# Kernel optimization log

Measured on AMD Instinct MI355X. Metric: run time of the kernel, lower is better.

The kernel has to match this reference:

```python
import jax, jax.numpy as jnp
import numpy as np

DIM = 1024
N_HEADS = 16
HEAD_DIM = DIM // N_HEADS
SCALE = 1.0 / HEAD_DIM ** 0.5


def setup_inputs() -> dict:
    key = jax.random.key(0)
    k1, k2, k3, k4, k5 = jax.random.split(key, 5)
    B, T = 4, 2048
    x = jax.random.normal(k1, (B, T, DIM), dtype=jnp.float32)
    # torch nn.Linear weights: y = x @ W.T + b
    w_qkv = jax.random.normal(k2, (3 * DIM, DIM), dtype=jnp.float32) * 0.02
    b_qkv = jax.random.normal(k3, (3 * DIM,), dtype=jnp.float32) * 0.02
    w_proj = jax.random.normal(k4, (DIM, DIM), dtype=jnp.float32) * 0.02
    b_proj = jax.random.normal(k5, (DIM,), dtype=jnp.float32) * 0.02
    return {"x": x, "w_qkv": w_qkv, "b_qkv": b_qkv, "w_proj": w_proj, "b_proj": b_proj}


def reference(x, w_qkv, b_qkv, w_proj, b_proj):
    B, T, D = x.shape
    qkv = x @ w_qkv.T + b_qkv                              # [B, T, 3D]
    qkv = qkv.reshape(B, T, 3, N_HEADS, HEAD_DIM)
    qkv = jnp.transpose(qkv, (2, 0, 3, 1, 4))              # [3, B, h, T, d]
    q, k, v = qkv[0], qkv[1], qkv[2]
    s = jnp.einsum('bhqd,bhkd->bhqk', q, k) * SCALE        # [B, h, T, T]
    attn = jax.nn.softmax(s, axis=-1)
    out = jnp.einsum('bhqk,bhkd->bqhd', attn, v)           # [B, T, h, d]
    out = out.reshape(B, T, D)
    return out @ w_proj.T + b_proj
```

## Files before the change

kernel.cpp:

```cpp
#include <hip/hip_runtime.h>
#include <stdint.h>

typedef short short8 __attribute__((ext_vector_type(8)));
typedef _Float16 half4 __attribute__((ext_vector_type(4)));
typedef _Float16 half8 __attribute__((ext_vector_type(8)));
typedef __fp16 fp16x2 __attribute__((ext_vector_type(2)));
typedef unsigned int uint2v __attribute__((ext_vector_type(2)));
typedef unsigned int uintx4 __attribute__((ext_vector_type(4)));
typedef float floatx4 __attribute__((ext_vector_type(4)));

#define LOG2E 1.44269504088896340736f
#define QSCALE (0.125f * LOG2E)

static __device__ __forceinline__ unsigned short f2bf(float f) {
  unsigned int u = __float_as_uint(f);
  u += 0x7fffu + ((u >> 16) & 1u);
  return (unsigned short)(u >> 16);
}

static __device__ __forceinline__ float fexp2(float x) {
#if __has_builtin(__builtin_amdgcn_exp2f)
  return __builtin_amdgcn_exp2f(x);
#else
  return exp2f(x);
#endif
}

#define GLD_LDS16(gp, lp)                                                      \
  __builtin_amdgcn_global_load_lds(                                            \
      (const __attribute__((address_space(1))) void*)(gp),                     \
      (__attribute__((address_space(3))) void*)(lp), 16, 0, 0)

__global__ __launch_bounds__(256) void cvt_f32_bf16(
    const float* __restrict__ in, unsigned short* __restrict__ out, int n) {
  int i = (blockIdx.x * 256 + threadIdx.x) * 4;
  if (i >= n) return;
  float4 v = *(const float4*)(in + i);
  ushort4 u;
  u.x = f2bf(v.x); u.y = f2bf(v.y); u.z = f2bf(v.z); u.w = f2bf(v.w);
  *(ushort4*)(out + i) = u;
}

template <int MODE>
__global__ __launch_bounds__(256, 2) void gemm_bt(
    const unsigned short* __restrict__ A, const unsigned short* __restrict__ Bm,
    const float* __restrict__ bias, float* __restrict__ outF,
    unsigned short* __restrict__ qo, unsigned short* __restrict__ ko,
    _Float16* __restrict__ vto, int M, int N, int K) {
  __shared__ unsigned short As[128 * 64];
  __shared__ unsigned short Bs[128 * 64];
  const int tid = threadIdx.x;
  const int w = tid >> 6, l = tid & 63;
  const int lr = l & 15, lg = l >> 4;
  const int nbn = N >> 7;
  const int nwg = gridDim.x;
  const int bid = blockIdx.x;
  const int cpx = nwg >> 3;
  const int swz = (bid & 7) * cpx + (bid >> 3);
  const int bm = swz / nbn, bn = swz % nbn;
  const int wm = w >> 1, wn = w & 1;

  floatx4 acc[4][4];
#pragma unroll
  for (int i = 0; i < 4; ++i)
#pragma unroll
    for (int j = 0; j < 4; ++j) acc[i][j] = (floatx4){0.f, 0.f, 0.f, 0.f};

  for (int k0 = 0; k0 < K; k0 += 64) {
#pragma unroll
    for (int i = 0; i < 4; ++i) {
      int c = i * 256 + tid;
      const unsigned short* ga =
          A + ((size_t)bm * 128 + (c >> 3)) * K + k0 + (c & 7) * 8;
      GLD_LDS16(ga, As + (size_t)(i * 256 + w * 64) * 8);
    }
#pragma unroll
    for (int i = 0; i < 4; ++i) {
      int c = i * 256 + tid;
      const unsigned short* gb =
          Bm + ((size_t)bn * 128 + (c >> 3)) * K + k0 + (c & 7) * 8;
      GLD_LDS16(gb, Bs + (size_t)(i * 256 + w * 64) * 8);
    }
    __syncthreads();
#pragma unroll
    for (int kk = 0; kk < 2; ++kk) {
      short8 af[4], bf[4];
#pragma unroll
      for (int i = 0; i < 4; ++i)
        af[i] = *(const short8*)&As[(wm * 64 + i * 16 + lr) * 64 + kk * 32 + lg * 8];
#pragma unroll
      for (int j = 0; j < 4; ++j)
        bf[j] = *(const short8*)&Bs[(wn * 64 + j * 16 + lr) * 64 + kk * 32 + lg * 8];
#pragma unroll
      for (int i = 0; i < 4; ++i)
#pragma unroll
        for (int j = 0; j < 4; ++j)
          acc[i][j] = __builtin_amdgcn_mfma_f32_16x16x32_bf16(af[i], bf[j],
                                                              acc[i][j], 0, 0, 0);
    }
    __syncthreads();
  }

#pragma unroll
  for (int i = 0; i < 4; ++i) {
    int row0 = bm * 128 + wm * 64 + i * 16 + lg * 4;
#pragma unroll
    for (int j = 0; j < 4; ++j) {
      int col = bn * 128 + wn * 64 + j * 16 + lr;
      float bv = bias[col];
#pragma unroll
      for (int jj = 0; jj < 4; ++jj) {
        float v = acc[i][j][jj] + bv;
        int r = row0 + jj;
        if (MODE == 0) {
          outF[(size_t)r * N + col] = v;
        } else {
          int three = col >> 10, cc = col & 1023;
          int h = cc >> 6, d = cc & 63;
          int b = r >> 11, t = r & 2047;
          if (three == 0)
            qo[(((size_t)(b * 16 + h)) * 2048 + t) * 64 + d] = f2bf(v * QSCALE);
          else if (three == 1)
            ko[(((size_t)(b * 16 + h)) * 2048 + t) * 64 + d] = f2bf(v);
          else
            vto[(((size_t)(b * 16 + h)) * 64 + d) * 2048 + t] = (_Float16)v;
        }
      }
    }
  }
}

__global__ __launch_bounds__(256, 3) void attn_fwd(
    const unsigned short* __restrict__ Qg, const unsigned short* __restrict__ Kg,
    const _Float16* __restrict__ VTg, unsigned short* __restrict__ Og) {
  __shared__ unsigned short Ks[2][64 * 64];
  __shared__ _Float16 Vs[2][64 * 64];

  const int bid0 = blockIdx.x;
  const int bid = (bid0 & 7) * 128 + (bid0 >> 3);
  const int bh = bid >> 4, qt = bid & 15;
  const int b = bh >> 4, hh = bh & 15;
  const int tid = threadIdx.x, w = tid >> 6, l = tid & 63;
  const int l4 = l & 15, g = l >> 4;
  const unsigned short* Q = Qg + (size_t)bh * (2048 * 64);
  const unsigned short* Kp = Kg + (size_t)bh * (2048 * 64);
  const _Float16* VT = VTg + (size_t)bh * (64 * 2048);
  const int qw = qt * 128 + w * 32;

  const int r0 = tid >> 3;
  const int s0 = (tid & 7) ^ (r0 & 7);
  const int kv0 = (r0 & 16) ? (((r0 & 15) >> 2) * 8 + 4 + (r0 & 3))
                            : ((r0 >> 2) * 8 + (r0 & 3));
  const unsigned short* kp0 = Kp + (size_t)kv0 * 64 + s0 * 8;
  const unsigned short* kp1 = Kp + (size_t)(kv0 + 32) * 64 + s0 * 8;
  const _Float16* vp0 = VT + (size_t)r0 * 2048 + s0 * 8;
  const _Float16* vp1 = VT + (size_t)(r0 + 32) * 2048 + s0 * 8;
  unsigned short* ksd0 = &Ks[0][tid * 8];
  unsigned short* ksd1 = &Ks[0][(256 + tid) * 8];
  _Float16* vsd0 = &Vs[0][tid * 8];
  _Float16* vsd1 = &Vs[0][(256 + tid) * 8];

#define STAGE(bufofs, tt)                                                     \
  do {                                                                        \
    GLD_LDS16(kp0 + (size_t)(tt) * 64, ksd0 + (bufofs) * 4096);               \
    GLD_LDS16(kp1 + (size_t)(tt) * 64, ksd1 + (bufofs) * 4096);               \
    GLD_LDS16(vp0 + (tt), vsd0 + (bufofs) * 4096);                            \
    GLD_LDS16(vp1 + (tt), vsd1 + (bufofs) * 4096);                            \
  } while (0)

  const int kb0 = l4 * 64 + ((g ^ (l4 & 7)) * 8);
  const int kb1 = l4 * 64 + (((4 + g) ^ (l4 & 7)) * 8);
  int vb[2];
#pragma unroll
  for (int B = 0; B < 2; ++B)
    vb[B] = l4 * 64 + (((B * 4 + g) ^ (l4 & 7)) * 8);

  short8 qf[2][2];
#pragma unroll
  for (int qs = 0; qs < 2; ++qs)
#pragma unroll
    for (int c = 0; c < 2; ++c)
      qf[qs][c] =
          *(const short8*)&Q[(size_t)(qw + qs * 16 + l4) * 64 + c * 32 + g * 8];

  floatx4 o[2][4];
#pragma unroll
  for (int qs = 0; qs < 2; ++qs)
#pragma unroll
    for (int db = 0; db < 4; ++db) o[qs][db] = (floatx4){0.f, 0.f, 0.f, 0.f};
  float m[2] = {-__builtin_inff(), -__builtin_inff()};
  float lp[2] = {0.f, 0.f};

  STAGE(0, 0);
  __syncthreads();

#pragma unroll 2
  for (int it = 0; it < 32; ++it) {
    const int cur = it & 1;
    if (it + 1 < 32) STAGE(cur ^ 1, (it + 1) * 64);

    floatx4 s[2][4];
#pragma unroll
    for (int f = 0; f < 4; ++f) {
      short8 kf0 = *(const short8*)&Ks[cur][kb0 + f * 1024];
      short8 kf1 = *(const short8*)&Ks[cur][kb1 + f * 1024];
      floatx4 z = (floatx4){0.f, 0.f, 0.f, 0.f};
      floatx4 t00 = __builtin_amdgcn_mfma_f32_16x16x32_bf16(kf0, qf[0][0], z, 0, 0, 0);
      s[0][f] = __builtin_amdgcn_mfma_f32_16x16x32_bf16(kf1, qf[0][1], t00, 0, 0, 0);
      floatx4 t10 = __builtin_amdgcn_mfma_f32_16x16x32_bf16(kf0, qf[1][0], z, 0, 0, 0);
      s[1][f] = __builtin_amdgcn_mfma_f32_16x16x32_bf16(kf1, qf[1][1], t10, 0, 0, 0);
    }

    uint2v pu[2][4];
#pragma unroll
    for (int qs = 0; qs < 2; ++qs) {
      float e[16];
      float rs = 0.f;
#pragma unroll
      for (int f = 0; f < 4; ++f)
#pragma unroll
        for (int jj = 0; jj < 4; ++jj) {
          float pv = fexp2(s[qs][f][jj] - m[qs]);
          e[f * 4 + jj] = pv;
          rs += pv;
        }

      if (!__all(rs <= 256.0f)) {
        float a0 = fmaxf(fmaxf(s[qs][0][0], s[qs][0][1]), fmaxf(s[qs][0][2], s[qs][0][3]));
        float a1 = fmaxf(fmaxf(s[qs][1][0], s[qs][1][1]), fmaxf(s[qs][1][2], s[qs][1][3]));
        float a2 = fmaxf(fmaxf(s[qs][2][0], s[qs][2][1]), fmaxf(s[qs][2][2], s[qs][2][3]));
        float a3 = fmaxf(fmaxf(s[qs][3][0], s[qs][3][1]), fmaxf(s[qs][3][2], s[qs][3][3]));
        float pp = fmaxf(fmaxf(a0, a1), fmaxf(a2, a3));
        pp = fmaxf(pp, __shfl_xor(pp, 16));
        pp = fmaxf(pp, __shfl_xor(pp, 32));
        float mo = m[qs];
        m[qs] = fmaxf(mo, pp);
        float al = fexp2(mo - m[qs]);
        lp[qs] *= al;
#pragma unroll
        for (int jj = 0; jj < 4; ++jj) {
          float alr = __shfl(al, g * 4 + jj);
          o[qs][0][jj] *= alr; o[qs][1][jj] *= alr;
          o[qs][2][jj] *= alr; o[qs][3][jj] *= alr;
        }
        rs = 0.f;
#pragma unroll
        for (int f = 0; f < 4; ++f)
#pragma unroll
          for (int jj = 0; jj < 4; ++jj) {
            float pv = fexp2(s[qs][f][jj] - m[qs]);
            e[f * 4 + jj] = pv;
            rs += pv;
          }
      }
      lp[qs] += rs;

#pragma unroll
      for (int f = 0; f < 4; ++f) {
        fp16x2 plo = __builtin_amdgcn_cvt_pkrtz(e[f * 4 + 0], e[f * 4 + 1]);
        fp16x2 phi = __builtin_amdgcn_cvt_pkrtz(e[f * 4 + 2], e[f * 4 + 3]);
        pu[qs][f].x = __builtin_bit_cast(unsigned int, plo);
        pu[qs][f].y = __builtin_bit_cast(unsigned int, phi);
      }
    }

#pragma unroll
    for (int B = 0; B < 2; ++B) {
      uintx4 ua0, ua1;
      ua0.x = pu[0][2 * B].x;     ua0.y = pu[0][2 * B].y;
      ua0.z = pu[0][2 * B + 1].x; ua0.w = pu[0][2 * B + 1].y;
      ua1.x = pu[1][2 * B].x;     ua1.y = pu[1][2 * B].y;
      ua1.z = pu[1][2 * B + 1].x; ua1.w = pu[1][2 * B + 1].y;
      half8 pa0 = __builtin_bit_cast(half8, ua0);
      half8 pa1 = __builtin_bit_cast(half8, ua1);
#pragma unroll
      for (int db = 0; db < 4; ++db) {
        half8 vf = *(const half8*)&Vs[cur][vb[B] + db * 1024];
        o[0][db] = __builtin_amdgcn_mfma_f32_16x16x32_f16(pa0, vf, o[0][db], 0, 0, 0);
        o[1][db] = __builtin_amdgcn_mfma_f32_16x16x32_f16(pa1, vf, o[1][db], 0, 0, 0);
      }
    }
    __syncthreads();
  }

#pragma unroll
  for (int qs = 0; qs < 2; ++qs) {
    float ls = lp[qs];
    ls += __shfl_xor(ls, 16);
    ls += __shfl_xor(ls, 32);
    float invq = 1.f / ls;
    float inv[4];
#pragma unroll
    for (int jj = 0; jj < 4; ++jj) inv[jj] = __shfl(invq, g * 4 + jj);
#pragma unroll
    for (int db = 0; db < 4; ++db)
#pragma unroll
      for (int jj = 0; jj < 4; ++jj)
        Og[((size_t)b * 2048 + qw + qs * 16 + g * 4 + jj) * 1024 + hh * 64 +
           db * 16 + l4] = f2bf(o[qs][db][jj] * inv[jj]);
  }
#undef STAGE
}

extern "C" void kernel_launch(void* const* d_in, const int* in_sizes, int n_in,
                              void* d_out, int out_size, void* d_ws, size_t ws_size,
                              hipStream_t stream) {
  const float* x = (const float*)d_in[0];
  const float* w_qkv = (const float*)d_in[1];
  const float* b_qkv = (const float*)d_in[2];
  const float* w_proj = (const float*)d_in[3];
  const float* b_proj = (const float*)d_in[4];
  float* out = (float*)d_out;

  char* p = (char*)d_ws;
  unsigned short* xb = (unsigned short*)p;     p += (size_t)8192 * 1024 * 2;
  unsigned short* wqkvb = (unsigned short*)p;  p += (size_t)3072 * 1024 * 2;
  unsigned short* wprojb = (unsigned short*)p; p += (size_t)1024 * 1024 * 2;
  unsigned short* qb = (unsigned short*)p;     p += (size_t)64 * 2048 * 64 * 2;
  unsigned short* kb = (unsigned short*)p;     p += (size_t)64 * 2048 * 64 * 2;
  _Float16* vtb = (_Float16*)p;                p += (size_t)64 * 64 * 2048 * 2;
  unsigned short* attnb = (unsigned short*)p;  p += (size_t)8192 * 1024 * 2;

  cvt_f32_bf16<<<dim3(8192), dim3(256), 0, stream>>>(x, xb, 8192 * 1024);
  cvt_f32_bf16<<<dim3(3072), dim3(256), 0, stream>>>(w_qkv, wqkvb, 3072 * 1024);
  cvt_f32_bf16<<<dim3(1024), dim3(256), 0, stream>>>(w_proj, wprojb, 1024 * 1024);

  gemm_bt<1><<<dim3(64 * 24), dim3(256), 0, stream>>>(
      xb, wqkvb, b_qkv, nullptr, qb, kb, vtb, 8192, 3072, 1024);

  attn_fwd<<<dim3(1024), dim3(256), 0, stream>>>(qb, kb, vtb, attnb);

  gemm_bt<0><<<dim3(64 * 8), dim3(256), 0, stream>>>(
      attnb, wprojb, b_proj, out, nullptr, nullptr, nullptr, 8192, 1024, 1024);
}
```

Before: 205.1 us.

## Rewrite GEMMs with 256x128 tiles, double-buffered swizzled LDS and prefetch

Replaces the single-buffer 128x128 GEMM with a 512-thread kernel computing 256x128 tiles, double-buffered LDS and an XOR swizzle on the k-slice index. Global-to-LDS loads for the next tiles are issued in two halves between the MFMA phases, with explicit vmcnt waits and raw barriers, so memory latency overlaps compute and bank conflicts drop. Setprio is raised around the MFMA blocks. The cost is more LDS and registers at one block per CU, and fewer blocks for the output projection.

```diff
diff --git a/kernel.cpp b/kernel.cpp
--- a/kernel.cpp
+++ b/kernel.cpp
@@ -30,6 +30,15 @@
   __builtin_amdgcn_global_load_lds(                                            \
       (const __attribute__((address_space(1))) void*)(gp),                     \
       (__attribute__((address_space(3))) void*)(lp), 16, 0, 0)
+
+#define FENCE() asm volatile("" ::: "memory")
+#define BARRIER()                                                              \
+  do {                                                                         \
+    FENCE();                                                                   \
+    __builtin_amdgcn_s_barrier();                                              \
+    FENCE();                                                                   \
+    __builtin_amdgcn_sched_barrier(0);                                         \
+  } while (0)
 
 __global__ __launch_bounds__(256) void cvt_f32_bf16(
     const float* __restrict__ in, unsigned short* __restrict__ out, int n) {
@@ -42,92 +51,139 @@
 }
 
 template <int MODE>
-__global__ __launch_bounds__(256, 2) void gemm_bt(
+__global__ __launch_bounds__(512, 1) void gemm_bt2(
     const unsigned short* __restrict__ A, const unsigned short* __restrict__ Bm,
     const float* __restrict__ bias, float* __restrict__ outF,
     unsigned short* __restrict__ qo, unsigned short* __restrict__ ko,
     _Float16* __restrict__ vto, int M, int N, int K) {
-  __shared__ unsigned short As[128 * 64];
-  __shared__ unsigned short Bs[128 * 64];
+  __shared__ unsigned short Asl[2][256 * 64];
+  __shared__ unsigned short Bsl[2][128 * 64];
   const int tid = threadIdx.x;
-  const int w = tid >> 6, l = tid & 63;
-  const int lr = l & 15, lg = l >> 4;
+  const int wid = tid >> 6, l = tid & 63;
+  const int l4 = l & 15, g = l >> 4;
+  const int wm = wid >> 2, wn = wid & 3;
   const int nbn = N >> 7;
-  const int nwg = gridDim.x;
-  const int bid = blockIdx.x;
+  const int nwg = gridDim.x, bid = blockIdx.x;
   const int cpx = nwg >> 3;
   const int swz = (bid & 7) * cpx + (bid >> 3);
   const int bm = swz / nbn, bn = swz % nbn;
-  const int wm = w >> 1, wn = w & 1;
-
-  floatx4 acc[4][4];
-#pragma unroll
-  for (int i = 0; i < 4; ++i)
-#pragma unroll
-    for (int j = 0; j < 4; ++j) acc[i][j] = (floatx4){0.f, 0.f, 0.f, 0.f};
-
-  for (int k0 = 0; k0 < K; k0 += 64) {
+  const int KT = K >> 6;
+
+  const int arow = tid >> 3;
+  const int asl = (tid & 7) ^ (arow & 7);
+  const unsigned short* Asrc = A + ((size_t)bm * 256 + arow) * K + asl * 8;
+  const unsigned short* Bsrc = Bm + ((size_t)bn * 128 + arow) * K + asl * 8;
+
+#define AISS(u, s, kt)                                                         \
+  GLD_LDS16(Asrc + (size_t)(u) * 64 * K + (kt) * 64, &Asl[s][((u) * 512 + tid) * 8])
+#define BISS(u, s, kt)                                                         \
+  GLD_LDS16(Bsrc + (size_t)(u) * 64 * K + (kt) * 64, &Bsl[s][((u) * 512 + tid) * 8])
+
+  const int sA0 = ((g) ^ (l4 & 7)) * 8;
+  const int sA1 = ((4 + g) ^ (l4 & 7)) * 8;
+  const int arb = (wm * 128 + l4) * 64;
+  const int brb = (wn * 32 + l4) * 64;
+
+  floatx4 acc[2][4][2];
+#pragma unroll
+  for (int qa = 0; qa < 2; ++qa)
+#pragma unroll
+    for (int i = 0; i < 4; ++i)
+#pragma unroll
+      for (int j = 0; j < 2; ++j) acc[qa][i][j] = (floatx4){0.f, 0.f, 0.f, 0.f};
+
+  AISS(0, 0, 0); AISS(1, 0, 0); AISS(2, 0, 0); AISS(3, 0, 0);
+  BISS(0, 0, 0); BISS(1, 0, 0);
+  AISS(0, 1, 1); AISS(2, 1, 1); BISS(0, 1, 1); BISS(1, 1, 1);
+  asm volatile("s_waitcnt vmcnt(4)" ::: "memory");
+  BARRIER();
+
+#pragma unroll 2
+  for (int t = 0; t < KT; ++t) {
+    const int s = t & 1;
+    if (t + 1 < KT) { AISS(1, s ^ 1, t + 1); AISS(3, s ^ 1, t + 1); }
+    short8 a0[4][2], bf[2][2];
 #pragma unroll
     for (int i = 0; i < 4; ++i) {
-      int c = i * 256 + tid;
-      const unsigned short* ga =
-          A + ((size_t)bm * 128 + (c >> 3)) * K + k0 + (c & 7) * 8;
-      GLD_LDS16(ga, As + (size_t)(i * 256 + w * 64) * 8);
-    }
+      a0[i][0] = *(const short8*)&Asl[s][arb + i * 1024 + sA0];
+      a0[i][1] = *(const short8*)&Asl[s][arb + i * 1024 + sA1];
+    }
+#pragma unroll
+    for (int j = 0; j < 2; ++j) {
+      bf[j][0] = *(const short8*)&Bsl[s][brb + j * 1024 + sA0];
+      bf[j][1] = *(const short8*)&Bsl[s][brb + j * 1024 + sA1];
+    }
+    __builtin_amdgcn_s_setprio(1);
+#pragma unroll
+    for (int i = 0; i < 4; ++i)
+#pragma unroll
+      for (int j = 0; j < 2; ++j) {
+        floatx4 tacc = __builtin_amdgcn_mfma_f32_16x16x32_bf16(
+            a0[i][0], bf[j][0], acc[0][i][j], 0, 0, 0);
+        acc[0][i][j] = __builtin_amdgcn_mfma_f32_16x16x32_bf16(
+            a0[i][1], bf[j][1], tacc, 0, 0, 0);
+      }
+    __builtin_amdgcn_s_setprio(0);
+    BARRIER();
+
+    if (t + 2 < KT) { AISS(0, s, t + 2); AISS(2, s, t + 2);
+                      BISS(0, s, t + 2); BISS(1, s, t + 2); }
+    short8 a1[4][2];
 #pragma unroll
     for (int i = 0; i < 4; ++i) {
-      int c = i * 256 + tid;
-      const unsigned short* gb =
-          Bm + ((size_t)bn * 128 + (c >> 3)) * K + k0 + (c & 7) * 8;
-      GLD_LDS16(gb, Bs + (size_t)(i * 256 + w * 64) * 8);
-    }
-    __syncthreads();
-#pragma unroll
-    for (int kk = 0; kk < 2; ++kk) {
-      short8 af[4], bf[4];
-#pragma unroll
-      for (int i = 0; i < 4; ++i)
-        af[i] = *(const short8*)&As[(wm * 64 + i * 16 + lr) * 64 + kk * 32 + lg * 8];
-#pragma unroll
-      for (int j = 0; j < 4; ++j)
-        bf[j] = *(const short8*)&Bs[(wn * 64 + j * 16 + lr) * 64 + kk * 32 + lg * 8];
-#pragma unroll
-      for (int i = 0; i < 4; ++i)
-#pragma unroll
-        for (int j = 0; j < 4; ++j)
-          acc[i][j] = __builtin_amdgcn_mfma_f32_16x16x32_bf16(af[i], bf[j],
-                                                              acc[i][j], 0, 0, 0);
-    }
-    __syncthreads();
+      a1[i][0] = *(const short8*)&Asl[s][arb + 64 * 64 + i * 1024 + sA0];
+      a1[i][1] = *(const short8*)&Asl[s][arb + 64 * 64 + i * 1024 + sA1];
+    }
+    __builtin_amdgcn_s_setprio(1);
+#pragma unroll
+    for (int i = 0; i < 4; ++i)
+#pragma unroll
+      for (int j = 0; j < 2; ++j) {
+        floatx4 tacc = __builtin_amdgcn_mfma_f32_16x16x32_bf16(
+            a1[i][0], bf[j][0], acc[1][i][j], 0, 0, 0);
+        acc[1][i][j] = __builtin_amdgcn_mfma_f32_16x16x32_bf16(
+            a1[i][1], bf[j][1], tacc, 0, 0, 0);
+      }
+    __builtin_amdgcn_s_setprio(0);
+    if (t + 2 < KT) {
+      asm volatile("s_waitcnt vmcnt(4)" ::: "memory");
+    } else if (t + 1 < KT) {
+      asm volatile("s_waitcnt vmcnt(0)" ::: "memory");
+    }
+    BARRIER();
   }
 
 #pragma unroll
-  for (int i = 0; i < 4; ++i) {
-    int row0 = bm * 128 + wm * 64 + i * 16 + lg * 4;
-#pragma unroll
-    for (int j = 0; j < 4; ++j) {
-      int col = bn * 128 + wn * 64 + j * 16 + lr;
-      float bv = bias[col];
-#pragma unroll
-      for (int jj = 0; jj < 4; ++jj) {
-        float v = acc[i][j][jj] + bv;
-        int r = row0 + jj;
-        if (MODE == 0) {
-          outF[(size_t)r * N + col] = v;
-        } else {
-          int three = col >> 10, cc = col & 1023;
-          int h = cc >> 6, d = cc & 63;
-          int b = r >> 11, t = r & 2047;
-          if (three == 0)
-            qo[(((size_t)(b * 16 + h)) * 2048 + t) * 64 + d] = f2bf(v * QSCALE);
-          else if (three == 1)
-            ko[(((size_t)(b * 16 + h)) * 2048 + t) * 64 + d] = f2bf(v);
-          else
-            vto[(((size_t)(b * 16 + h)) * 64 + d) * 2048 + t] = (_Float16)v;
+  for (int qa = 0; qa < 2; ++qa)
+#pragma unroll
+    for (int i = 0; i < 4; ++i) {
+      int row0 = bm * 256 + wm * 128 + qa * 64 + i * 16 + g * 4;
+#pragma unroll
+      for (int j = 0; j < 2; ++j) {
+        int col = bn * 128 + wn * 32 + j * 16 + l4;
+        float bv = bias[col];
+#pragma unroll
+        for (int jj = 0; jj < 4; ++jj) {
+          float v = acc[qa][i][j][jj] + bv;
+          int r = row0 + jj;
+          if (MODE == 0) {
+            outF[(size_t)r * N + col] = v;
+          } else {
+            int three = col >> 10, cc = col & 1023;
+            int h = cc >> 6, d = cc & 63;
+            int b = r >> 11, tt = r & 2047;
+            if (three == 0)
+              qo[(((size_t)(b * 16 + h)) * 2048 + tt) * 64 + d] = f2bf(v * QSCALE);
+            else if (three == 1)
+              ko[(((size_t)(b * 16 + h)) * 2048 + tt) * 64 + d] = f2bf(v);
+            else
+              vto[(((size_t)(b * 16 + h)) * 64 + d) * 2048 + tt] = (_Float16)v;
+          }
         }
       }
     }
-  }
+#undef AISS
+#undef BISS
 }
 
 __global__ __launch_bounds__(256, 3) void attn_fwd(
@@ -325,11 +381,11 @@
   cvt_f32_bf16<<<dim3(3072), dim3(256), 0, stream>>>(w_qkv, wqkvb, 3072 * 1024);
   cvt_f32_bf16<<<dim3(1024), dim3(256), 0, stream>>>(w_proj, wprojb, 1024 * 1024);
 
-  gemm_bt<1><<<dim3(64 * 24), dim3(256), 0, stream>>>(
+  gemm_bt2<1><<<dim3(32 * 24), dim3(512), 0, stream>>>(
       xb, wqkvb, b_qkv, nullptr, qb, kb, vtb, 8192, 3072, 1024);
 
   attn_fwd<<<dim3(1024), dim3(256), 0, stream>>>(qb, kb, vtb, attnb);
 
-  gemm_bt<0><<<dim3(64 * 8), dim3(256), 0, stream>>>(
+  gemm_bt2<0><<<dim3(32 * 8), dim3(512), 0, stream>>>(
       attnb, wprojb, b_proj, out, nullptr, nullptr, nullptr, 8192, 1024, 1024);
 }
```

After: 229.6 us. +11.9%, slower.
